# Performance work log

Hardware: AMD Instinct MI355X
Metric: run time of the kernel (lower is better)

Reference implementation:

```python
import jax, jax.numpy as jnp
import numpy as np

NEG_SLOPE = 0.2  # PyG GATConv LeakyReLU slope
N_NODES = 50000
N_EDGES = 800000
F_IN, HID, HEADS, N_CLS = 166, 64, 8, 2


def setup_inputs() -> dict:
    key = jax.random.key(0)
    ks = jax.random.split(key, 16)
    s = 0.1
    return {
        "x": jax.random.normal(ks[0], (N_NODES, F_IN), jnp.float32),
        "edge_index": jax.random.randint(ks[1], (2, N_EDGES), 0, N_NODES, jnp.int64),
        "W1": jax.random.normal(ks[2], (F_IN, HEADS * HID), jnp.float32) * s,
        "a_src1": jax.random.normal(ks[3], (HEADS, HID), jnp.float32) * s,
        "a_dst1": jax.random.normal(ks[4], (HEADS, HID), jnp.float32) * s,
        "b1": jnp.zeros((HEADS * HID,), jnp.float32),
        # conv_final: 512 -> 64, 1 head, mean (concat=False)
        "W2": jax.random.normal(ks[5], (HEADS * HID, HID), jnp.float32) * s,
        "a_src2": jax.random.normal(ks[6], (1, HID), jnp.float32) * s,
        "a_dst2": jax.random.normal(ks[7], (1, HID), jnp.float32) * s,
        "b2": jnp.zeros((HID,), jnp.float32),
        # classifier MLP 64 -> 64 -> 2
        "Wc1": jax.random.normal(ks[8], (HID, HID), jnp.float32) * s,
        "bc1": jnp.zeros((HID,), jnp.float32),
        "Wc2": jax.random.normal(ks[9], (HID, N_CLS), jnp.float32) * s,
        "bc2": jnp.zeros((N_CLS,), jnp.float32),
    }


def gat_layer(x, src, dst, W, a_src, a_dst, b, concat):
    """PyG-style GATConv (eval mode, self-loops already in src/dst)."""
    N = x.shape[0]
    H, C = a_src.shape
    xp = (x @ W).reshape(N, H, C)                 # [N,H,C] projected features
    al_src = jnp.sum(xp * a_src, axis=-1)         # [N,H]
    al_dst = jnp.sum(xp * a_dst, axis=-1)         # [N,H]
    e = jax.nn.leaky_relu(al_src[src] + al_dst[dst], NEG_SLOPE)  # [E,H]
    # segment softmax over incoming edges of each target node
    m = jax.ops.segment_max(e, dst, num_segments=N)
    ex = jnp.exp(e - m[dst])
    denom = jax.ops.segment_sum(ex, dst, num_segments=N)
    alpha = ex / denom[dst]                       # [E,H]
    out = jax.ops.segment_sum(alpha[:, :, None] * xp[src], dst, num_segments=N)  # [N,H,C]
    out = out.reshape(N, H * C) if concat else out.mean(axis=1)
    return out + b


def reference(x, edge_index, W1, a_src1, a_dst1, b1, W2, a_src2, a_dst2, b2, Wc1, bc1, Wc2, bc2):
    N = x.shape[0]
    loops = jnp.arange(N, dtype=edge_index.dtype)
    src = jnp.concatenate([edge_index[0], loops])  # add self-loops (PyG default)
    dst = jnp.concatenate([edge_index[1], loops])
    h = jax.nn.elu(gat_layer(x, src, dst, W1, a_src1, a_dst1, b1, concat=True))
    h = gat_layer(h, src, dst, W2, a_src2, a_dst2, b2, concat=False)
    h = jax.nn.relu(h @ Wc1 + bc1)
    return h @ Wc2 + bc2
```

## Files before the change

kernel.cpp:

```cpp
#include <hip/hip_runtime.h>

#define NN   50000
#define E0   800000
#define ET   850000
#define FIN  166
#define KP1  192
#define HID  64
#define NH   8
#define F1   512
#define SCHUNK 52
#define DEGPAD (1024*SCHUNK)

typedef __attribute__((ext_vector_type(8))) short short8;
typedef __attribute__((ext_vector_type(4))) float f32x4;
typedef __attribute__((ext_vector_type(4))) int int4v;

__device__ __forceinline__ float bf2f(unsigned short u){
  unsigned int x = ((unsigned int)u) << 16;
  return __builtin_bit_cast(float, x);
}
__device__ __forceinline__ unsigned short f2bf(float f){
  unsigned int x = __builtin_bit_cast(unsigned int, f);
  x += 0x7FFFu + ((x >> 16) & 1u);
  return (unsigned short)(x >> 16);
}

__global__ __launch_bounds__(256) void k_pad_x(const float* __restrict__ x,
                                               unsigned short* __restrict__ xpad){
  const long long total = (long long)NN * KP1;
  for (long long i = (long long)blockIdx.x*256 + threadIdx.x; i < total;
       i += (long long)gridDim.x*256){
    int n = (int)(i / KP1), k = (int)(i % KP1);
    float v = (k < FIN) ? x[(size_t)n*FIN + k] : 0.f;
    xpad[i] = f2bf(v);
  }
}

__global__ __launch_bounds__(256) void k_prep(const float* __restrict__ W1,
                                              const float* __restrict__ W2,
                                              unsigned short* __restrict__ W1t,
                                              unsigned short* __restrict__ W2t){
  const int tot1 = 512*KP1, tot2 = HID*F1;
  int i = blockIdx.x*256 + threadIdx.x;
  if (i < tot1){
    int col = i / KP1, k = i % KP1;
    float v = (k < FIN) ? W1[(size_t)k*512 + col] : 0.f;
    W1t[i] = f2bf(v);
  } else if (i < tot1 + tot2){
    int j = i - tot1;
    int col = j / F1, k = j % F1;
    W2t[j] = f2bf(W2[(size_t)k*HID + col]);
  }
}

__global__ __launch_bounds__(256) void k_hist(const int* __restrict__ ei,
                                              int* __restrict__ deg){
  for (int e = blockIdx.x*256 + threadIdx.x; e < ET; e += gridDim.x*256){
    int dst = (e < E0) ? ei[E0 + e] : (e - E0);
    atomicAdd(&deg[dst], 1);
  }
}

__global__ __launch_bounds__(1024) void k_scan(const int* __restrict__ deg,
                                               int* __restrict__ offs){
  __shared__ int sums[1024];
  int t = threadIdx.x;
  int base = t * SCHUNK;
  int4v v[13];
  int loc = 0;
  #pragma unroll
  for (int c = 0; c < 13; c++){
    v[c] = *(const int4v*)(deg + base + c*4);
    loc += v[c].x + v[c].y + v[c].z + v[c].w;
  }
  sums[t] = loc; __syncthreads();
  for (int off = 1; off < 1024; off <<= 1){
    int s = (t >= off) ? sums[t - off] : 0;
    __syncthreads();
    sums[t] += s;
    __syncthreads();
  }
  int run = sums[t] - loc;
  #pragma unroll
  for (int c = 0; c < 13; c++){
    int i0 = base + c*4;
    if (i0 + 0 < NN) offs[i0 + 0] = run;  run += v[c].x;
    if (i0 + 1 < NN) offs[i0 + 1] = run;  run += v[c].y;
    if (i0 + 2 < NN) offs[i0 + 2] = run;  run += v[c].z;
    if (i0 + 3 < NN) offs[i0 + 3] = run;  run += v[c].w;
  }
  if (t == 1023) offs[NN] = sums[1023];
}

__global__ __launch_bounds__(256) void k_scatter(const int* __restrict__ ei,
                                                 const int* __restrict__ offs,
                                                 int* __restrict__ cur,
                                                 int* __restrict__ esrc){
  for (int e = blockIdx.x*256 + threadIdx.x; e < ET; e += gridDim.x*256){
    int src, dst;
    if (e < E0){ src = ei[e]; dst = ei[E0 + e]; }
    else       { src = e - E0; dst = src; }
    int pos = offs[dst] + atomicAdd(&cur[dst], 1);
    esrc[pos] = src;
  }
}

template<int KSTEPS, bool OUT_BF16, bool DO_AL, int ALH>
__global__ __launch_bounds__(256) void k_gemm(const unsigned short* __restrict__ A,
                                              int lda, int M,
                                              const unsigned short* __restrict__ Bt,
                                              void* __restrict__ C, int ldc,
                                              const float* __restrict__ a_s,
                                              const float* __restrict__ a_d,
                                              float* __restrict__ als,
                                              float* __restrict__ ald){
  __shared__ unsigned short As[64][40];
  __shared__ unsigned short Bs[64][40];
  __shared__ float redS[64][2];
  __shared__ float redD[64][2];
  const int m0 = blockIdx.x * 64;
  const int n0 = blockIdx.y * 64;
  const int t  = threadIdx.x;
  const int wid = t >> 6, l = t & 63;
  const int wr = wid >> 1, wc = wid & 1;
  const int lr = l & 15, ksl = (l >> 4) * 8;

  f32x4 acc[2][2];
  #pragma unroll
  for (int m = 0; m < 2; m++)
    #pragma unroll
    for (int n = 0; n < 2; n++)
      #pragma unroll
      for (int j = 0; j < 4; j++) acc[m][n][j] = 0.f;

  const int arow = t >> 2, akc = (t & 3) * 8;

  for (int s = 0; s < KSTEPS; s++){
    const int kk = s * 32;
    short8 av;
    #pragma unroll
    for (int j = 0; j < 8; j++) av[j] = 0;
    int gr = m0 + arow;
    if (gr < M) av = *(const short8*)(A + (size_t)gr*lda + kk + akc);
    *(short8*)&As[arow][akc] = av;
    short8 bv = *(const short8*)(Bt + (size_t)(n0 + arow)*lda + kk + akc);
    *(short8*)&Bs[arow][akc] = bv;
    __syncthreads();

    short8 af[2], bf_[2];
    #pragma unroll
    for (int m = 0; m < 2; m++) af[m]  = *(const short8*)&As[wr*32 + m*16 + lr][ksl];
    #pragma unroll
    for (int n = 0; n < 2; n++) bf_[n] = *(const short8*)&Bs[wc*32 + n*16 + lr][ksl];
    #pragma unroll
    for (int m = 0; m < 2; m++)
      #pragma unroll
      for (int n = 0; n < 2; n++)
        acc[m][n] = __builtin_amdgcn_mfma_f32_16x16x32_bf16(af[m], bf_[n], acc[m][n], 0, 0, 0);
    __syncthreads();
  }

  #pragma unroll
  for (int m = 0; m < 2; m++)
    #pragma unroll
    for (int n = 0; n < 2; n++)
      #pragma unroll
      for (int j = 0; j < 4; j++){
        int gr = m0 + wr*32 + m*16 + (l >> 4)*4 + j;
        int gc = n0 + wc*32 + n*16 + lr;
        if (gr < M){
          if (OUT_BF16) ((unsigned short*)C)[(size_t)gr*ldc + gc] = f2bf(acc[m][n][j]);
          else          ((float*)C)[(size_t)gr*ldc + gc]          = acc[m][n][j];
        }
      }

  if (DO_AL){
    const float* asp = a_s + (ALH > 1 ? (int)blockIdx.y*64 : 0);
    const float* adp = a_d + (ALH > 1 ? (int)blockIdx.y*64 : 0);
    float c0 = asp[wc*32 + lr],      c1 = asp[wc*32 + 16 + lr];
    float d0 = adp[wc*32 + lr],      d1 = adp[wc*32 + 16 + lr];
    #pragma unroll
    for (int m = 0; m < 2; m++)
      #pragma unroll
      for (int j = 0; j < 4; j++){
        float ps = acc[m][0][j]*c0 + acc[m][1][j]*c1;
        float pd = acc[m][0][j]*d0 + acc[m][1][j]*d1;
        #pragma unroll
        for (int o = 1; o < 16; o <<= 1){
          ps += __shfl_xor(ps, o, 64);
          pd += __shfl_xor(pd, o, 64);
        }
        if (lr == 0){
          int rl = wr*32 + m*16 + (l >> 4)*4 + j;
          redS[rl][wc] = ps;
          redD[rl][wc] = pd;
        }
      }
    __syncthreads();
    if (t < 64){
      int gr = m0 + t;
      if (gr < M){
        float s = redS[t][0] + redS[t][1];
        float d = redD[t][0] + redD[t][1];
        s = fminf(fmaxf(s, -30.f), 30.f);
        d = fminf(fmaxf(d, -30.f), 30.f);
        int head = (ALH > 1) ? blockIdx.y : 0;
        als[(size_t)gr*ALH + head] = s;
        ald[(size_t)gr*ALH + head] = d;
      }
    }
  }
}

__global__ __launch_bounds__(256) void k_agg1(const int* __restrict__ offs,
                                              const int* __restrict__ esrc,
                                              const unsigned short* __restrict__ xp1,
                                              const float* __restrict__ als,
                                              const float* __restrict__ ald,
                                              const float* __restrict__ b1,
                                              unsigned short* __restrict__ h1){
  int w = (blockIdx.x*256 + threadIdx.x) >> 6;
  int l = threadIdx.x & 63;
  if (w >= NN) return;
  int h = l >> 3;
  int f0 = l * 8;
  float ad = ald[w*NH + h];
  int s0 = offs[w], s1 = offs[w+1];
  float accA[8], accB[8];
  #pragma unroll
  for (int j = 0; j < 8; j++){ accA[j] = 0.f; accB[j] = 0.f; }
  float denA = 0.f, denB = 0.f;
  int i = s0;
  for (; i + 2 <= s1; i += 2){
    int sA = esrc[i], sB = esrc[i+1];
    float eA = als[sA*NH + h] + ad;
    float eB = als[sB*NH + h] + ad;
    eA = fmaxf(eA, 0.2f*eA);
    eB = fmaxf(eB, 0.2f*eB);
    float wA = __expf(eA), wB = __expf(eB);
    short8 vA = *(const short8*)(xp1 + (size_t)sA*F1 + f0);
    short8 vB = *(const short8*)(xp1 + (size_t)sB*F1 + f0);
    denA += wA; denB += wB;
    #pragma unroll
    for (int j = 0; j < 8; j++){
      accA[j] = fmaf(wA, bf2f((unsigned short)vA[j]), accA[j]);
      accB[j] = fmaf(wB, bf2f((unsigned short)vB[j]), accB[j]);
    }
  }
  if (i < s1){
    int sA = esrc[i];
    float eA = als[sA*NH + h] + ad;
    eA = fmaxf(eA, 0.2f*eA);
    float wA = __expf(eA);
    short8 vA = *(const short8*)(xp1 + (size_t)sA*F1 + f0);
    denA += wA;
    #pragma unroll
    for (int j = 0; j < 8; j++) accA[j] = fmaf(wA, bf2f((unsigned short)vA[j]), accA[j]);
  }
  float inv = 1.f / (denA + denB);
  #pragma unroll
  for (int j = 0; j < 8; j++){
    float o = (accA[j] + accB[j])*inv + b1[f0 + j];
    o = o > 0.f ? o : expm1f(o);
    h1[(size_t)w*F1 + f0 + j] = f2bf(o);
  }
}

__global__ __launch_bounds__(256) void k_agg2(const int* __restrict__ offs,
                                              const int* __restrict__ esrc,
                                              const float* __restrict__ xp2,
                                              const float* __restrict__ als,
                                              const float* __restrict__ ald,
                                              const float* __restrict__ b2,
                                              const float* __restrict__ Wc1,
                                              const float* __restrict__ bc1,
                                              const float* __restrict__ Wc2,
                                              const float* __restrict__ bc2,
                                              float* __restrict__ out){
  int w = (blockIdx.x*256 + threadIdx.x) >> 6;
  int l = threadIdx.x & 63;
  if (w >= NN) return;
  float ad = ald[w];
  int s0 = offs[w], s1 = offs[w+1];
  float accA = 0.f, accB = 0.f, denA = 0.f, denB = 0.f;
  int i = s0;
  for (; i + 2 <= s1; i += 2){
    int sA = esrc[i], sB = esrc[i+1];
    float eA = als[sA] + ad;
    float eB = als[sB] + ad;
    eA = fmaxf(eA, 0.2f*eA);
    eB = fmaxf(eB, 0.2f*eB);
    float wA = __expf(eA), wB = __expf(eB);
    float xA = xp2[(size_t)sA*HID + l];
    float xB = xp2[(size_t)sB*HID + l];
    denA += wA; denB += wB;
    accA = fmaf(wA, xA, accA);
    accB = fmaf(wB, xB, accB);
  }
  if (i < s1){
    int sA = esrc[i];
    float eA = als[sA] + ad;
    eA = fmaxf(eA, 0.2f*eA);
    float wA = __expf(eA);
    denA += wA;
    accA = fmaf(wA, xp2[(size_t)sA*HID + l], accA);
  }
  float h2 = (accA + accB) / (denA + denB) + b2[l];
  float r = 0.f;
  #pragma unroll
  for (int k = 0; k < 64; k++){
    float hk = __shfl(h2, k, 64);
    r = fmaf(hk, Wc1[k*HID + l], r);
  }
  r += bc1[l];
  r = fmaxf(r, 0.f);
  float p0 = r * Wc2[l*2 + 0];
  float p1 = r * Wc2[l*2 + 1];
  #pragma unroll
  for (int o = 1; o < 64; o <<= 1){
    p0 += __shfl_xor(p0, o, 64);
    p1 += __shfl_xor(p1, o, 64);
  }
  if (l == 0){
    out[(size_t)w*2 + 0] = p0 + bc2[0];
    out[(size_t)w*2 + 1] = p1 + bc2[1];
  }
}

extern "C" void kernel_launch(void* const* d_in, const int* in_sizes, int n_in,
                              void* d_out, int out_size, void* d_ws, size_t ws_size,
                              hipStream_t stream){
  const float* x   = (const float*)d_in[0];
  const int*   ei  = (const int*)  d_in[1];
  const float* W1  = (const float*)d_in[2];
  const float* as1 = (const float*)d_in[3];
  const float* ad1 = (const float*)d_in[4];
  const float* b1  = (const float*)d_in[5];
  const float* W2  = (const float*)d_in[6];
  const float* as2 = (const float*)d_in[7];
  const float* ad2 = (const float*)d_in[8];
  const float* b2  = (const float*)d_in[9];
  const float* Wc1 = (const float*)d_in[10];
  const float* bc1 = (const float*)d_in[11];
  const float* Wc2 = (const float*)d_in[12];
  const float* bc2 = (const float*)d_in[13];
  float* out = (float*)d_out;

  char* p = (char*)d_ws; size_t off = 0;
  auto alloc = [&](size_t b){ void* r = p + off; off = (off + b + 255) & ~(size_t)255; return r; };
  unsigned short* xpad = (unsigned short*)alloc((size_t)NN*KP1*2);
  unsigned short* W1t  = (unsigned short*)alloc((size_t)512*KP1*2);
  unsigned short* W2t  = (unsigned short*)alloc((size_t)HID*F1*2);
  unsigned short* xp1  = (unsigned short*)alloc((size_t)NN*F1*2);
  unsigned short* h1   = (unsigned short*)alloc((size_t)NN*F1*2);
  float* xp2  = (float*)alloc((size_t)NN*HID*4);
  float* als1 = (float*)alloc((size_t)NN*NH*4);
  float* ald1 = (float*)alloc((size_t)NN*NH*4);
  float* als2 = (float*)alloc((size_t)NN*4);
  float* ald2 = (float*)alloc((size_t)NN*4);
  int* deg  = (int*)alloc((size_t)DEGPAD*4);
  int* cur  = (int*)alloc((size_t)NN*4);
  int* offs = (int*)alloc((size_t)(NN+1)*4);
  int* esrc = (int*)alloc((size_t)ET*4);

  hipMemsetAsync(deg, 0, (size_t)DEGPAD*4, stream);
  hipMemsetAsync(cur, 0, (size_t)NN*4, stream);

  k_pad_x<<<4096, 256, 0, stream>>>(x, xpad);
  k_prep<<<512, 256, 0, stream>>>(W1, W2, W1t, W2t);
  k_hist<<<(ET + 255)/256, 256, 0, stream>>>(ei, deg);
  k_scan<<<1, 1024, 0, stream>>>(deg, offs);
  k_scatter<<<(ET + 255)/256, 256, 0, stream>>>(ei, offs, cur, esrc);

  k_gemm<6, true, true, 8><<<dim3(782, 8), 256, 0, stream>>>(
      xpad, KP1, NN, W1t, (void*)xp1, F1, as1, ad1, als1, ald1);
  k_agg1<<<12500, 256, 0, stream>>>(offs, esrc, xp1, als1, ald1, b1, h1);

  k_gemm<16, false, true, 1><<<dim3(782, 1), 256, 0, stream>>>(
      h1, F1, NN, W2t, (void*)xp2, HID, as2, ad2, als2, ald2);
  k_agg2<<<12500, 256, 0, stream>>>(offs, esrc, xp2, als2, ald2, b2, Wc1, bc1, Wc2, bc2, out);
}
```

Before: 404.4 us.

## Merge prep kernels, enlarge GEMM tiles, store xp2 as bf16, batch edge loads

Result: faster. 394.0 us (-2.6%).

```diff
diff --git a/kernel.cpp b/kernel.cpp
--- a/kernel.cpp
+++ b/kernel.cpp
@@ -14,6 +14,7 @@
 typedef __attribute__((ext_vector_type(8))) short short8;
 typedef __attribute__((ext_vector_type(4))) float f32x4;
 typedef __attribute__((ext_vector_type(4))) int int4v;
+typedef unsigned short ush;
 
 __device__ __forceinline__ float bf2f(unsigned short u){
   unsigned int x = ((unsigned int)u) << 16;
@@ -25,37 +26,31 @@
   return (unsigned short)(x >> 16);
 }
 
-__global__ __launch_bounds__(256) void k_pad_x(const float* __restrict__ x,
-                                               unsigned short* __restrict__ xpad){
-  const long long total = (long long)NN * KP1;
-  for (long long i = (long long)blockIdx.x*256 + threadIdx.x; i < total;
-       i += (long long)gridDim.x*256){
-    int n = (int)(i / KP1), k = (int)(i % KP1);
-    float v = (k < FIN) ? x[(size_t)n*FIN + k] : 0.f;
-    xpad[i] = f2bf(v);
-  }
-}
-
-__global__ __launch_bounds__(256) void k_prep(const float* __restrict__ W1,
-                                              const float* __restrict__ W2,
-                                              unsigned short* __restrict__ W1t,
-                                              unsigned short* __restrict__ W2t){
-  const int tot1 = 512*KP1, tot2 = HID*F1;
+__global__ __launch_bounds__(256) void k_prep_all(const float* __restrict__ x,
+                                                  const float* __restrict__ W1,
+                                                  const float* __restrict__ W2,
+                                                  const int* __restrict__ ei,
+                                                  ush* __restrict__ xpad,
+                                                  ush* __restrict__ W1t,
+                                                  ush* __restrict__ W2t,
+                                                  int* __restrict__ deg){
+  const int T0 = NN*KP1;
+  const int T1 = T0 + 512*KP1;
+  const int T2 = T1 + HID*F1;
+  const int T3 = T2 + ET;
   int i = blockIdx.x*256 + threadIdx.x;
-  if (i < tot1){
-    int col = i / KP1, k = i % KP1;
-    float v = (k < FIN) ? W1[(size_t)k*512 + col] : 0.f;
-    W1t[i] = f2bf(v);
-  } else if (i < tot1 + tot2){
-    int j = i - tot1;
-    int col = j / F1, k = j % F1;
+  if (i >= T3) return;
+  if (i < T0){
+    int n = i / KP1, k = i % KP1;
+    xpad[i] = f2bf(k < FIN ? x[(size_t)n*FIN + k] : 0.f);
+  } else if (i < T1){
+    int j = i - T0; int col = j / KP1, k = j % KP1;
+    W1t[j] = f2bf(k < FIN ? W1[(size_t)k*512 + col] : 0.f);
+  } else if (i < T2){
+    int j = i - T1; int col = j / F1, k = j % F1;
     W2t[j] = f2bf(W2[(size_t)k*HID + col]);
-  }
-}
-
-__global__ __launch_bounds__(256) void k_hist(const int* __restrict__ ei,
-                                              int* __restrict__ deg){
-  for (int e = blockIdx.x*256 + threadIdx.x; e < ET; e += gridDim.x*256){
+  } else {
+    int e = i - T2;
     int dst = (e < E0) ? ei[E0 + e] : (e - E0);
     atomicAdd(&deg[dst], 1);
   }
@@ -105,120 +100,205 @@
   }
 }
 
-template<int KSTEPS, bool OUT_BF16, bool DO_AL, int ALH>
-__global__ __launch_bounds__(256) void k_gemm(const unsigned short* __restrict__ A,
-                                              int lda, int M,
-                                              const unsigned short* __restrict__ Bt,
-                                              void* __restrict__ C, int ldc,
-                                              const float* __restrict__ a_s,
-                                              const float* __restrict__ a_d,
-                                              float* __restrict__ als,
-                                              float* __restrict__ ald){
-  __shared__ unsigned short As[64][40];
-  __shared__ unsigned short Bs[64][40];
-  __shared__ float redS[64][2];
-  __shared__ float redD[64][2];
-  const int m0 = blockIdx.x * 64;
-  const int n0 = blockIdx.y * 64;
-  const int t  = threadIdx.x;
-  const int wid = t >> 6, l = t & 63;
-  const int wr = wid >> 1, wc = wid & 1;
-  const int lr = l & 15, ksl = (l >> 4) * 8;
-
-  f32x4 acc[2][2];
+__global__ __launch_bounds__(256) void k_gemm1(const ush* __restrict__ xpad,
+                                               const ush* __restrict__ W1t,
+                                               const float* __restrict__ a_s,
+                                               const float* __restrict__ a_d,
+                                               ush* __restrict__ xp1,
+                                               float* __restrict__ als,
+                                               float* __restrict__ ald){
+  __shared__ ush As[128][40];
+  __shared__ ush Bs[128][40];
+  const int m0 = blockIdx.x*128, n0 = blockIdx.y*128;
+  const int t = threadIdx.x, wid = t>>6, l = t&63;
+  const int wr = wid>>1, wc = wid&1;
+  const int lr = l&15, ksl = (l>>4)*8;
+  const int srow = t>>1, sc = (t&1)*16;
+
+  f32x4 acc[4][4];
+  #pragma unroll
+  for (int m = 0; m < 4; m++)
+    #pragma unroll
+    for (int n = 0; n < 4; n++)
+      #pragma unroll
+      for (int j = 0; j < 4; j++) acc[m][n][j] = 0.f;
+
+  const int gr = m0 + srow;
+  const ush* Ap = xpad + (size_t)gr*KP1 + sc;
+  const ush* Bp = W1t + (size_t)(n0 + srow)*KP1 + sc;
+
+  for (int s = 0; s < 6; s++){
+    const int kk = s*32;
+    short8 a0, a1;
+    #pragma unroll
+    for (int j = 0; j < 8; j++){ a0[j] = 0; a1[j] = 0; }
+    if (gr < NN){ a0 = *(const short8*)(Ap + kk); a1 = *(const short8*)(Ap + kk + 8); }
+    short8 b0 = *(const short8*)(Bp + kk);
+    short8 b1 = *(const short8*)(Bp + kk + 8);
+    *(short8*)&As[srow][sc]   = a0;
+    *(short8*)&As[srow][sc+8] = a1;
+    *(short8*)&Bs[srow][sc]   = b0;
+    *(short8*)&Bs[srow][sc+8] = b1;
+    __syncthreads();
+    short8 af[4], bfr[4];
+    #pragma unroll
+    for (int m = 0; m < 4; m++) af[m]  = *(const short8*)&As[wr*64 + m*16 + lr][ksl];
+    #pragma unroll
+    for (int n = 0; n < 4; n++) bfr[n] = *(const short8*)&Bs[wc*64 + n*16 + lr][ksl];
+    #pragma unroll
+    for (int m = 0; m < 4; m++)
+      #pragma unroll
+      for (int n = 0; n < 4; n++)
+        acc[m][n] = __builtin_amdgcn_mfma_f32_16x16x32_bf16(af[m], bfr[n], acc[m][n], 0, 0, 0);
+    __syncthreads();
+  }
+
+  #pragma unroll
+  for (int m = 0; m < 4; m++)
+    #pragma unroll
+    for (int n = 0; n < 4; n++)
+      #pragma unroll
+      for (int j = 0; j < 4; j++){
+        int row = m0 + wr*64 + m*16 + (l>>4)*4 + j;
+        int col = n0 + wc*64 + n*16 + lr;
+        if (row < NN) xp1[(size_t)row*F1 + col] = f2bf(acc[m][n][j]);
+      }
+
+  const int head = blockIdx.y*2 + wc;
+  float asv[4], adv[4];
+  #pragma unroll
+  for (int n = 0; n < 4; n++){
+    asv[n] = a_s[head*64 + n*16 + lr];
+    adv[n] = a_d[head*64 + n*16 + lr];
+  }
+  #pragma unroll
+  for (int m = 0; m < 4; m++)
+    #pragma unroll
+    for (int j = 0; j < 4; j++){
+      float ps = 0.f, pd = 0.f;
+      #pragma unroll
+      for (int n = 0; n < 4; n++){
+        ps = fmaf(acc[m][n][j], asv[n], ps);
+        pd = fmaf(acc[m][n][j], adv[n], pd);
+      }
+      #pragma unroll
+      for (int o = 1; o < 16; o <<= 1){
+        ps += __shfl_xor(ps, o, 64);
+        pd += __shfl_xor(pd, o, 64);
+      }
+      if (lr == 0){
+        int row = m0 + wr*64 + m*16 + (l>>4)*4 + j;
+        if (row < NN){
+          als[(size_t)row*NH + head] = fminf(fmaxf(ps, -30.f), 30.f);
+          ald[(size_t)row*NH + head] = fminf(fmaxf(pd, -30.f), 30.f);
+        }
+      }
+    }
+}
+
+__global__ __launch_bounds__(256) void k_gemm2(const ush* __restrict__ h1,
+                                               const ush* __restrict__ W2t,
+                                               const float* __restrict__ a_s,
+                                               const float* __restrict__ a_d,
+                                               ush* __restrict__ xp2,
+                                               float* __restrict__ als,
+                                               float* __restrict__ ald){
+  __shared__ ush As[128][40];
+  __shared__ ush Bs[64][40];
+  const int m0 = blockIdx.x*128;
+  const int t = threadIdx.x, wid = t>>6, l = t&63;
+  const int lr = l&15, ksl = (l>>4)*8;
+  const int srow = t>>1, sc = (t&1)*16;
+
+  f32x4 acc[2][4];
   #pragma unroll
   for (int m = 0; m < 2; m++)
     #pragma unroll
-    for (int n = 0; n < 2; n++)
+    for (int n = 0; n < 4; n++)
       #pragma unroll
       for (int j = 0; j < 4; j++) acc[m][n][j] = 0.f;
 
-  const int arow = t >> 2, akc = (t & 3) * 8;
-
-  for (int s = 0; s < KSTEPS; s++){
-    const int kk = s * 32;
-    short8 av;
-    #pragma unroll
-    for (int j = 0; j < 8; j++) av[j] = 0;
-    int gr = m0 + arow;
-    if (gr < M) av = *(const short8*)(A + (size_t)gr*lda + kk + akc);
-    *(short8*)&As[arow][akc] = av;
-    short8 bv = *(const short8*)(Bt + (size_t)(n0 + arow)*lda + kk + akc);
-    *(short8*)&Bs[arow][akc] = bv;
-    __syncthreads();
-
-    short8 af[2], bf_[2];
-    #pragma unroll
-    for (int m = 0; m < 2; m++) af[m]  = *(const short8*)&As[wr*32 + m*16 + lr][ksl];
-    #pragma unroll
-    for (int n = 0; n < 2; n++) bf_[n] = *(const short8*)&Bs[wc*32 + n*16 + lr][ksl];
+  const int gr = m0 + srow;
+  const ush* Ap = h1 + (size_t)gr*F1 + sc;
+  const ush* Bp = W2t + (size_t)srow*F1 + sc;
+
+  for (int s = 0; s < 16; s++){
+    const int kk = s*32;
+    short8 a0, a1;
+    #pragma unroll
+    for (int j = 0; j < 8; j++){ a0[j] = 0; a1[j] = 0; }
+    if (gr < NN){ a0 = *(const short8*)(Ap + kk); a1 = *(const short8*)(Ap + kk + 8); }
+    *(short8*)&As[srow][sc]   = a0;
+    *(short8*)&As[srow][sc+8] = a1;
+    if (t < 128){
+      short8 b0 = *(const short8*)(Bp + kk);
+      short8 b1 = *(const short8*)(Bp + kk + 8);
+      *(short8*)&Bs[srow][sc]   = b0;
+      *(short8*)&Bs[srow][sc+8] = b1;
+    }
+    __syncthreads();
+    short8 af[2], bfr[4];
+    #pragma unroll
+    for (int m = 0; m < 2; m++) af[m]  = *(const short8*)&As[wid*32 + m*16 + lr][ksl];
+    #pragma unroll
+    for (int n = 0; n < 4; n++) bfr[n] = *(const short8*)&Bs[n*16 + lr][ksl];
     #pragma unroll
     for (int m = 0; m < 2; m++)
       #pragma unroll
-      for (int n = 0; n < 2; n++)
-        acc[m][n] = __builtin_amdgcn_mfma_f32_16x16x32_bf16(af[m], bf_[n], acc[m][n], 0, 0, 0);
+      for (int n = 0; n < 4; n++)
+        acc[m][n] = __builtin_amdgcn_mfma_f32_16x16x32_bf16(af[m], bfr[n], acc[m][n], 0, 0, 0);
     __syncthreads();
   }
 
   #pragma unroll
   for (int m = 0; m < 2; m++)
     #pragma unroll
-    for (int n = 0; n < 2; n++)
+    for (int n = 0; n < 4; n++)
       #pragma unroll
       for (int j = 0; j < 4; j++){
-        int gr = m0 + wr*32 + m*16 + (l >> 4)*4 + j;
-        int gc = n0 + wc*32 + n*16 + lr;
-        if (gr < M){
-          if (OUT_BF16) ((unsigned short*)C)[(size_t)gr*ldc + gc] = f2bf(acc[m][n][j]);
-          else          ((float*)C)[(size_t)gr*ldc + gc]          = acc[m][n][j];
+        int row = m0 + wid*32 + m*16 + (l>>4)*4 + j;
+        int col = n*16 + lr;
+        if (row < NN) xp2[(size_t)row*HID + col] = f2bf(acc[m][n][j]);
+      }
+
+  float asv[4], adv[4];
+  #pragma unroll
+  for (int n = 0; n < 4; n++){
+    asv[n] = a_s[n*16 + lr];
+    adv[n] = a_d[n*16 + lr];
+  }
+  #pragma unroll
+  for (int m = 0; m < 2; m++)
+    #pragma unroll
+    for (int j = 0; j < 4; j++){
+      float ps = 0.f, pd = 0.f;
+      #pragma unroll
+      for (int n = 0; n < 4; n++){
+        ps = fmaf(acc[m][n][j], asv[n], ps);
+        pd = fmaf(acc[m][n][j], adv[n], pd);
+      }
+      #pragma unroll
+      for (int o = 1; o < 16; o <<= 1){
+        ps += __shfl_xor(ps, o, 64);
+        pd += __shfl_xor(pd, o, 64);
+      }
+      if (lr == 0){
+        int row = m0 + wid*32 + m*16 + (l>>4)*4 + j;
+        if (row < NN){
+          als[row] = fminf(fmaxf(ps, -30.f), 30.f);
+          ald[row] = fminf(fmaxf(pd, -30.f), 30.f);
         }
       }
-
-  if (DO_AL){
-    const float* asp = a_s + (ALH > 1 ? (int)blockIdx.y*64 : 0);
-    const float* adp = a_d + (ALH > 1 ? (int)blockIdx.y*64 : 0);
-    float c0 = asp[wc*32 + lr],      c1 = asp[wc*32 + 16 + lr];
-    float d0 = adp[wc*32 + lr],      d1 = adp[wc*32 + 16 + lr];
-    #pragma unroll
-    for (int m = 0; m < 2; m++)
-      #pragma unroll
-      for (int j = 0; j < 4; j++){
-        float ps = acc[m][0][j]*c0 + acc[m][1][j]*c1;
-        float pd = acc[m][0][j]*d0 + acc[m][1][j]*d1;
-        #pragma unroll
-        for (int o = 1; o < 16; o <<= 1){
-          ps += __shfl_xor(ps, o, 64);
-          pd += __shfl_xor(pd, o, 64);
-        }
-        if (lr == 0){
-          int rl = wr*32 + m*16 + (l >> 4)*4 + j;
-          redS[rl][wc] = ps;
-          redD[rl][wc] = pd;
-        }
-      }
-    __syncthreads();
-    if (t < 64){
-      int gr = m0 + t;
-      if (gr < M){
-        float s = redS[t][0] + redS[t][1];
-        float d = redD[t][0] + redD[t][1];
-        s = fminf(fmaxf(s, -30.f), 30.f);
-        d = fminf(fmaxf(d, -30.f), 30.f);
-        int head = (ALH > 1) ? blockIdx.y : 0;
-        als[(size_t)gr*ALH + head] = s;
-        ald[(size_t)gr*ALH + head] = d;
-      }
-    }
-  }
+    }
 }
 
 __global__ __launch_bounds__(256) void k_agg1(const int* __restrict__ offs,
                                               const int* __restrict__ esrc,
-                                              const unsigned short* __restrict__ xp1,
+                                              const ush* __restrict__ xp1,
                                               const float* __restrict__ als,
                                               const float* __restrict__ ald,
                                               const float* __restrict__ b1,
-                                              unsigned short* __restrict__ h1){
+                                              ush* __restrict__ h1){
   int w = (blockIdx.x*256 + threadIdx.x) >> 6;
   int l = threadIdx.x & 63;
   if (w >= NN) return;
@@ -229,46 +309,61 @@
   float accA[8], accB[8];
   #pragma unroll
   for (int j = 0; j < 8; j++){ accA[j] = 0.f; accB[j] = 0.f; }
-  float denA = 0.f, denB = 0.f;
-  int i = s0;
-  for (; i + 2 <= s1; i += 2){
-    int sA = esrc[i], sB = esrc[i+1];
-    float eA = als[sA*NH + h] + ad;
-    float eB = als[sB*NH + h] + ad;
-    eA = fmaxf(eA, 0.2f*eA);
-    eB = fmaxf(eB, 0.2f*eB);
-    float wA = __expf(eA), wB = __expf(eB);
-    short8 vA = *(const short8*)(xp1 + (size_t)sA*F1 + f0);
-    short8 vB = *(const short8*)(xp1 + (size_t)sB*F1 + f0);
-    denA += wA; denB += wB;
-    #pragma unroll
-    for (int j = 0; j < 8; j++){
-      accA[j] = fmaf(wA, bf2f((unsigned short)vA[j]), accA[j]);
-      accB[j] = fmaf(wB, bf2f((unsigned short)vB[j]), accB[j]);
-    }
-  }
-  if (i < s1){
-    int sA = esrc[i];
-    float eA = als[sA*NH + h] + ad;
-    eA = fmaxf(eA, 0.2f*eA);
-    float wA = __expf(eA);
-    short8 vA = *(const short8*)(xp1 + (size_t)sA*F1 + f0);
-    denA += wA;
-    #pragma unroll
-    for (int j = 0; j < 8; j++) accA[j] = fmaf(wA, bf2f((unsigned short)vA[j]), accA[j]);
-  }
-  float inv = 1.f / (denA + denB);
-  #pragma unroll
-  for (int j = 0; j < 8; j++){
-    float o = (accA[j] + accB[j])*inv + b1[f0 + j];
+  float den = 0.f;
+
+  for (int base = s0; base < s1; base += 64){
+    int cnt = min(64, s1 - base);
+    int myE = (base + l < s1) ? esrc[base + l] : 0;
+    int j = 0;
+    for (; j + 4 <= cnt; j += 4){
+      int sA = __shfl(myE, j,   64);
+      int sB = __shfl(myE, j+1, 64);
+      int sC = __shfl(myE, j+2, 64);
+      int sD = __shfl(myE, j+3, 64);
+      float eA = als[sA*NH + h] + ad;
+      float eB = als[sB*NH + h] + ad;
+      float eC = als[sC*NH + h] + ad;
+      float eD = als[sD*NH + h] + ad;
+      eA = fmaxf(eA, 0.2f*eA); eB = fmaxf(eB, 0.2f*eB);
+      eC = fmaxf(eC, 0.2f*eC); eD = fmaxf(eD, 0.2f*eD);
+      float wA = __expf(eA), wB = __expf(eB), wC = __expf(eC), wD = __expf(eD);
+      short8 vA = *(const short8*)(xp1 + (size_t)sA*F1 + f0);
+      short8 vB = *(const short8*)(xp1 + (size_t)sB*F1 + f0);
+      short8 vC = *(const short8*)(xp1 + (size_t)sC*F1 + f0);
+      short8 vD = *(const short8*)(xp1 + (size_t)sD*F1 + f0);
+      den += (wA + wB) + (wC + wD);
+      #pragma unroll
+      for (int jj = 0; jj < 8; jj++){
+        accA[jj] = fmaf(wA, bf2f((ush)vA[jj]), accA[jj]);
+        accB[jj] = fmaf(wB, bf2f((ush)vB[jj]), accB[jj]);
+        accA[jj] = fmaf(wC, bf2f((ush)vC[jj]), accA[jj]);
+        accB[jj] = fmaf(wD, bf2f((ush)vD[jj]), accB[jj]);
+      }
+    }
+    for (; j < cnt; j++){
+      int sA = __shfl(myE, j, 64);
+      float eA = als[sA*NH + h] + ad;
+      eA = fmaxf(eA, 0.2f*eA);
+      float wA = __expf(eA);
+      short8 vA = *(const short8*)(xp1 + (size_t)sA*F1 + f0);
+      den += wA;
+      #pragma unroll
+      for (int jj = 0; jj < 8; jj++)
+        accA[jj] = fmaf(wA, bf2f((ush)vA[jj]), accA[jj]);
+    }
+  }
+  float inv = 1.f / den;
+  #pragma unroll
+  for (int jj = 0; jj < 8; jj++){
+    float o = (accA[jj] + accB[jj])*inv + b1[f0 + jj];
     o = o > 0.f ? o : expm1f(o);
-    h1[(size_t)w*F1 + f0 + j] = f2bf(o);
+    h1[(size_t)w*F1 + f0 + jj] = f2bf(o);
   }
 }
 
 __global__ __launch_bounds__(256) void k_agg2(const int* __restrict__ offs,
                                               const int* __restrict__ esrc,
-                                              const float* __restrict__ xp2,
+                                              const ush* __restrict__ xp2,
                                               const float* __restrict__ als,
                                               const float* __restrict__ ald,
                                               const float* __restrict__ b2,
@@ -282,30 +377,39 @@
   if (w >= NN) return;
   float ad = ald[w];
   int s0 = offs[w], s1 = offs[w+1];
-  float accA = 0.f, accB = 0.f, denA = 0.f, denB = 0.f;
-  int i = s0;
-  for (; i + 2 <= s1; i += 2){
-    int sA = esrc[i], sB = esrc[i+1];
-    float eA = als[sA] + ad;
-    float eB = als[sB] + ad;
-    eA = fmaxf(eA, 0.2f*eA);
-    eB = fmaxf(eB, 0.2f*eB);
-    float wA = __expf(eA), wB = __expf(eB);
-    float xA = xp2[(size_t)sA*HID + l];
-    float xB = xp2[(size_t)sB*HID + l];
-    denA += wA; denB += wB;
-    accA = fmaf(wA, xA, accA);
-    accB = fmaf(wB, xB, accB);
-  }
-  if (i < s1){
-    int sA = esrc[i];
-    float eA = als[sA] + ad;
-    eA = fmaxf(eA, 0.2f*eA);
-    float wA = __expf(eA);
-    denA += wA;
-    accA = fmaf(wA, xp2[(size_t)sA*HID + l], accA);
-  }
-  float h2 = (accA + accB) / (denA + denB) + b2[l];
+  float accA = 0.f, accB = 0.f, den = 0.f;
+
+  for (int base = s0; base < s1; base += 64){
+    int cnt = min(64, s1 - base);
+    int myE = (base + l < s1) ? esrc[base + l] : 0;
+    int j = 0;
+    for (; j + 4 <= cnt; j += 4){
+      int sA = __shfl(myE, j,   64);
+      int sB = __shfl(myE, j+1, 64);
+      int sC = __shfl(myE, j+2, 64);
+      int sD = __shfl(myE, j+3, 64);
+      float eA = als[sA] + ad, eB = als[sB] + ad, eC = als[sC] + ad, eD = als[sD] + ad;
+      eA = fmaxf(eA, 0.2f*eA); eB = fmaxf(eB, 0.2f*eB);
+      eC = fmaxf(eC, 0.2f*eC); eD = fmaxf(eD, 0.2f*eD);
+      float wA = __expf(eA), wB = __expf(eB), wC = __expf(eC), wD = __expf(eD);
+      float xA = bf2f(xp2[(size_t)sA*HID + l]);
+      float xB = bf2f(xp2[(size_t)sB*HID + l]);
+      float xC = bf2f(xp2[(size_t)sC*HID + l]);
+      float xD = bf2f(xp2[(size_t)sD*HID + l]);
+      den += (wA + wB) + (wC + wD);
+      accA = fmaf(wA, xA, accA); accB = fmaf(wB, xB, accB);
+      accA = fmaf(wC, xC, accA); accB = fmaf(wD, xD, accB);
+    }
+    for (; j < cnt; j++){
+      int sA = __shfl(myE, j, 64);
+      float eA = als[sA] + ad;
+      eA = fmaxf(eA, 0.2f*eA);
+      float wA = __expf(eA);
+      den += wA;
+      accA = fmaf(wA, bf2f(xp2[(size_t)sA*HID + l]), accA);
+    }
+  }
+  float h2 = (accA + accB) / den + b2[l];
   float r = 0.f;
   #pragma unroll
   for (int k = 0; k < 64; k++){
@@ -348,12 +452,12 @@
 
   char* p = (char*)d_ws; size_t off = 0;
   auto alloc = [&](size_t b){ void* r = p + off; off = (off + b + 255) & ~(size_t)255; return r; };
-  unsigned short* xpad = (unsigned short*)alloc((size_t)NN*KP1*2);
-  unsigned short* W1t  = (unsigned short*)alloc((size_t)512*KP1*2);
-  unsigned short* W2t  = (unsigned short*)alloc((size_t)HID*F1*2);
-  unsigned short* xp1  = (unsigned short*)alloc((size_t)NN*F1*2);
-  unsigned short* h1   = (unsigned short*)alloc((size_t)NN*F1*2);
-  float* xp2  = (float*)alloc((size_t)NN*HID*4);
+  ush* xpad = (ush*)alloc((size_t)NN*KP1*2);
+  ush* W1t  = (ush*)alloc((size_t)512*KP1*2);
+  ush* W2t  = (ush*)alloc((size_t)HID*F1*2);
+  ush* xp1  = (ush*)alloc((size_t)NN*F1*2);
+  ush* h1   = (ush*)alloc((size_t)NN*F1*2);
+  ush* xp2  = (ush*)alloc((size_t)NN*HID*2);
   float* als1 = (float*)alloc((size_t)NN*NH*4);
   float* ald1 = (float*)alloc((size_t)NN*NH*4);
   float* als2 = (float*)alloc((size_t)NN*4);
@@ -366,17 +470,14 @@
   hipMemsetAsync(deg, 0, (size_t)DEGPAD*4, stream);
   hipMemsetAsync(cur, 0, (size_t)NN*4, stream);
 
-  k_pad_x<<<4096, 256, 0, stream>>>(x, xpad);
-  k_prep<<<512, 256, 0, stream>>>(W1, W2, W1t, W2t);
-  k_hist<<<(ET + 255)/256, 256, 0, stream>>>(ei, deg);
+  const int T3 = NN*KP1 + 512*KP1 + HID*F1 + ET;
+  k_prep_all<<<(T3 + 255)/256, 256, 0, stream>>>(x, W1, W2, ei, xpad, W1t, W2t, deg);
   k_scan<<<1, 1024, 0, stream>>>(deg, offs);
   k_scatter<<<(ET + 255)/256, 256, 0, stream>>>(ei, offs, cur, esrc);
 
-  k_gemm<6, true, true, 8><<<dim3(782, 8), 256, 0, stream>>>(
-      xpad, KP1, NN, W1t, (void*)xp1, F1, as1, ad1, als1, ald1);
+  k_gemm1<<<dim3(391, 4), 256, 0, stream>>>(xpad, W1t, as1, ad1, xp1, als1, ald1);
   k_agg1<<<12500, 256, 0, stream>>>(offs, esrc, xp1, als1, ald1, b1, h1);
 
-  k_gemm<16, false, true, 1><<<dim3(782, 1), 256, 0, stream>>>(
-      h1, F1, NN, W2t, (void*)xp2, HID, as2, ad2, als2, ald2);
+  k_gemm2<<<391, 256, 0, stream>>>(h1, W2t, as2, ad2, xp2, als2, ald2);
   k_agg2<<<12500, 256, 0, stream>>>(offs, esrc, xp2, als2, ald2, b2, Wc1, bc1, Wc2, bc2, out);
 }
```
